# Performance work log

Hardware: AMD Instinct MI355X
Metric: run time of the kernel (lower is better)

The kernel has to match this reference:

```python
import jax, jax.numpy as jnp
import numpy as np

SIM_THRESHOLD = 0.9


def setup_inputs() -> dict:
    key = jax.random.key(0)
    k1, k2 = jax.random.split(key)
    # patches: b * c * num * ws * ws  (b=2, c=8, num=1024, ws=3) -> n = 16384
    patches = jax.random.normal(k1, (2, 8, 1024, 3, 3), dtype=jnp.float32)
    # db: m * ws * ws
    db = jax.random.normal(k2, (16384, 3, 3), dtype=jnp.float32)
    return {"patches": patches, "db": db}


def reference(patches, db):
    ws = patches.shape[-1]
    p = patches.reshape(-1, ws, ws)          # [n, ws, ws]
    n = p.shape[0]
    m = db.shape[0]
    pf = p.reshape(n, -1)                    # [n, ws*ws]
    df = db.reshape(m, -1)                   # [m, ws*ws]
    dot = pf @ df.T                          # [n, m], tiny K=ws*ws -> memory bound
    norm_n = jnp.linalg.norm(pf, axis=1, keepdims=True)   # [n, 1]
    norm_m = jnp.linalg.norm(df, axis=1, keepdims=True)   # [m, 1]
    cos = dot / (norm_n * norm_m.T)          # [n, m] cosine similarity
    # patch kept only if dissimilar to EVERY db entry
    mask = jnp.all(cos < SIM_THRESHOLD, axis=1)            # [n] bool
    # jit-friendly fixed-shape compaction: zero out rejected patches instead of
    # dropping rows (original does db = cat(db, patches[mask]))
    filtered = jnp.where(mask[:, None, None], p, jnp.zeros((), p.dtype))
    return jnp.concatenate([db.reshape(-1, ws, ws), filtered], axis=0)  # [m+n, ws, ws]
```

## Files before the change

### kernel.cpp

```cpp
#include <hip/hip_runtime.h>

#define NPATCH 16384
#define NDB    16384
#define WS9    9
#define KP     16
#define JCH    16
#define CHUNK  (NDB / JCH)
#define TILES  (CHUNK / 32)
#define BAND_LO 0.8998f
#define BAND_HI 0.9002f

typedef short bf16x8 __attribute__((ext_vector_type(8)));
typedef float f32x16 __attribute__((ext_vector_type(16)));

__device__ __forceinline__ float np_norm9(const float* v) {
#pragma clang fp contract(off)
    float q0 = v[0] * v[0], q1 = v[1] * v[1], q2 = v[2] * v[2], q3 = v[3] * v[3];
    float q4 = v[4] * v[4], q5 = v[5] * v[5], q6 = v[6] * v[6], q7 = v[7] * v[7];
    float q8 = v[8] * v[8];
    float s = ((q0 + q1) + (q2 + q3)) + ((q4 + q5) + (q6 + q7));
    s = s + q8;
    return sqrtf(s);
}

__device__ __forceinline__ unsigned enc_f(float f) {
    unsigned u = __float_as_uint(f);
    return (u & 0x80000000u) ? ~u : (u | 0x80000000u);
}
__device__ __forceinline__ float dec_f(unsigned k) {
    return __uint_as_float((k & 0x80000000u) ? (k & 0x7fffffffu) : ~k);
}

__device__ __forceinline__ unsigned short f2bf(float x) {
    unsigned u = __float_as_uint(x);
    return (unsigned short)((u + 0x7fffu + ((u >> 16) & 1u)) >> 16);
}
__device__ __forceinline__ float bf2f(unsigned short h) {
    return __uint_as_float(((unsigned)h) << 16);
}

__global__ __launch_bounds__(256) void k_prep(const float* __restrict__ patches,
                                              const float* __restrict__ db,
                                              unsigned short* __restrict__ pn_hi,
                                              unsigned short* __restrict__ pn_lo,
                                              unsigned short* __restrict__ dn_hi,
                                              unsigned short* __restrict__ dn_lo,
                                              unsigned* __restrict__ maxenc,
                                              int* __restrict__ band_count) {
    int j = blockIdx.x * 256 + threadIdx.x;
    if (j == 0) *band_count = 0;
    maxenc[j] = 0u;

    float d[WS9];
#pragma unroll
    for (int k = 0; k < WS9; k++) d[k] = db[j * WS9 + k];
    float invd = 1.0f / np_norm9(d);
#pragma unroll
    for (int k = 0; k < KP; k++) {
        float v = (k < WS9) ? d[k] * invd : 0.0f;
        unsigned short h = f2bf(v);
        dn_hi[j * KP + k] = h;
        dn_lo[j * KP + k] = f2bf(v - bf2f(h));
    }

    float p[WS9];
#pragma unroll
    for (int k = 0; k < WS9; k++) p[k] = patches[j * WS9 + k];
    float invp = 1.0f / np_norm9(p);
#pragma unroll
    for (int k = 0; k < KP; k++) {
        float v = (k < WS9) ? p[k] * invp : 0.0f;
        unsigned short h = f2bf(v);
        pn_hi[j * KP + k] = h;
        pn_lo[j * KP + k] = f2bf(v - bf2f(h));
    }
}

__global__ __launch_bounds__(256) void k_phase1(const unsigned short* __restrict__ pn_hi,
                                                const unsigned short* __restrict__ pn_lo,
                                                const unsigned short* __restrict__ dn_hi,
                                                const unsigned short* __restrict__ dn_lo,
                                                unsigned* __restrict__ maxenc) {
    int lane = threadIdx.x & 63;
    int wave = threadIdx.x >> 6;
    int col = lane & 31;
    int half = lane >> 5;
    int i0 = blockIdx.x * 256 + wave * 64;

    const bf16x8* Bh = (const bf16x8*)pn_hi;
    const bf16x8* Bl = (const bf16x8*)pn_lo;
    bf16x8 b_hi0 = Bh[(i0 + col) * 2 + half];
    bf16x8 b_lo0 = Bl[(i0 + col) * 2 + half];
    bf16x8 b_hi1 = Bh[(i0 + 32 + col) * 2 + half];
    bf16x8 b_lo1 = Bl[(i0 + 32 + col) * 2 + half];

    int jrow = blockIdx.y * CHUNK + col;
    const bf16x8* Ah = (const bf16x8*)dn_hi + (size_t)jrow * 2 + half;
    const bf16x8* Al = (const bf16x8*)dn_lo + (size_t)jrow * 2 + half;

    f32x16 zc = {0.f,0.f,0.f,0.f,0.f,0.f,0.f,0.f,0.f,0.f,0.f,0.f,0.f,0.f,0.f,0.f};
    float rm0 = -3.0e38f, rm1 = -3.0e38f;

    bf16x8 a_h = Ah[0], a_l = Al[0];
#pragma unroll 2
    for (int t = 0; t < TILES; ++t) {
        bf16x8 a_h_n = a_h, a_l_n = a_l;
        if (t + 1 < TILES) {
            a_h_n = Ah[(t + 1) * 64];
            a_l_n = Al[(t + 1) * 64];
        }
        f32x16 acc0 = __builtin_amdgcn_mfma_f32_32x32x16_bf16(a_h, b_hi0, zc, 0, 0, 0);
        acc0 = __builtin_amdgcn_mfma_f32_32x32x16_bf16(a_h, b_lo0, acc0, 0, 0, 0);
        acc0 = __builtin_amdgcn_mfma_f32_32x32x16_bf16(a_l, b_hi0, acc0, 0, 0, 0);
        f32x16 acc1 = __builtin_amdgcn_mfma_f32_32x32x16_bf16(a_h, b_hi1, zc, 0, 0, 0);
        acc1 = __builtin_amdgcn_mfma_f32_32x32x16_bf16(a_h, b_lo1, acc1, 0, 0, 0);
        acc1 = __builtin_amdgcn_mfma_f32_32x32x16_bf16(a_l, b_hi1, acc1, 0, 0, 0);
#pragma unroll
        for (int r = 0; r < 16; ++r) {
            rm0 = fmaxf(rm0, acc0[r]);
            rm1 = fmaxf(rm1, acc1[r]);
        }
        a_h = a_h_n;
        a_l = a_l_n;
    }
    rm0 = fmaxf(rm0, __shfl_xor(rm0, 32, 64));
    rm1 = fmaxf(rm1, __shfl_xor(rm1, 32, 64));
    unsigned e = half ? enc_f(rm1) : enc_f(rm0);
    int ti = half ? (i0 + 32 + col) : (i0 + col);
    atomicMax(&maxenc[ti], e);
}

__global__ __launch_bounds__(256) void k_combine(const float* __restrict__ patches,
                                                 const float* __restrict__ db,
                                                 const unsigned* __restrict__ maxenc,
                                                 float* __restrict__ out,
                                                 int* __restrict__ band_list,
                                                 int* __restrict__ band_count) {
    int i = blockIdx.x * 256 + threadIdx.x;
#pragma unroll
    for (int k = 0; k < WS9; k++) out[i * WS9 + k] = db[i * WS9 + k];
    float cosmax = dec_f(maxenc[i]);
    if (cosmax >= BAND_LO && cosmax < BAND_HI) {
        int idx = atomicAdd(band_count, 1);
        band_list[idx] = i;
        return;
    }
    int hit = (cosmax >= BAND_HI) ? 1 : 0;
#pragma unroll
    for (int k = 0; k < WS9; k++)
        out[(NDB + i) * WS9 + k] = hit ? 0.0f : patches[i * WS9 + k];
}

__global__ __launch_bounds__(256) void k_phase2(const float* __restrict__ patches,
                                                const float* __restrict__ db,
                                                const int* __restrict__ band_list,
                                                const int* __restrict__ band_count,
                                                float* __restrict__ out) {
    __shared__ float sp[WS9];
    __shared__ float snp;
    __shared__ int shit;
    int nb = *band_count;
    for (int idx = blockIdx.x; idx < nb; idx += gridDim.x) {
        int i = band_list[idx];
        if (threadIdx.x == 0) {
            float p[WS9];
            for (int k = 0; k < WS9; k++) { p[k] = patches[i * WS9 + k]; sp[k] = p[k]; }
            snp = np_norm9(p);
            shit = 0;
        }
        __syncthreads();
        float p[WS9];
#pragma unroll
        for (int k = 0; k < WS9; k++) p[k] = sp[k];
        float npn = snp;
        int hit = 0;
        for (int j = (int)threadIdx.x; j < NDB; j += 256) {
            float d[WS9];
#pragma unroll
            for (int k = 0; k < WS9; k++) d[k] = db[j * WS9 + k];
            float dot = 0.0f;
#pragma unroll
            for (int k = 0; k < WS9; k++) dot = fmaf(p[k], d[k], dot);
            float nd = np_norm9(d);
            float cs = dot / (npn * nd);
            if (!((double)cs < 0.9)) hit = 1;
        }
        if (hit) atomicOr(&shit, 1);
        __syncthreads();
        int m = shit;
        if (threadIdx.x < WS9)
            out[(NDB + i) * WS9 + threadIdx.x] = m ? 0.0f : sp[threadIdx.x];
        __syncthreads();
    }
}

extern "C" void kernel_launch(void* const* d_in, const int* in_sizes, int n_in,
                              void* d_out, int out_size, void* d_ws, size_t ws_size,
                              hipStream_t stream) {
    const float* patches = (const float*)d_in[0];
    const float* db      = (const float*)d_in[1];
    float* out = (float*)d_out;

    char* wsb = (char*)d_ws;
    unsigned*       maxenc     = (unsigned*)wsb;
    int*            band_list  = (int*)(wsb + (size_t)64 * 1024);
    int*            band_count = (int*)(wsb + (size_t)128 * 1024);
    unsigned short* pn_hi      = (unsigned short*)(wsb + (size_t)128 * 1024 + 16);
    unsigned short* pn_lo      = pn_hi + (size_t)NPATCH * KP;
    unsigned short* dn_hi      = pn_lo + (size_t)NPATCH * KP;
    unsigned short* dn_lo      = dn_hi + (size_t)NDB * KP;

    k_prep<<<dim3(NDB / 256), dim3(256), 0, stream>>>(patches, db, pn_hi, pn_lo,
                                                      dn_hi, dn_lo, maxenc, band_count);
    k_phase1<<<dim3(NPATCH / 256, JCH), dim3(256), 0, stream>>>(pn_hi, pn_lo,
                                                                dn_hi, dn_lo, maxenc);
    k_combine<<<dim3(NPATCH / 256), dim3(256), 0, stream>>>(patches, db, maxenc,
                                                            out, band_list, band_count);
    k_phase2<<<dim3(512), dim3(256), 0, stream>>>(patches, db, band_list, band_count, out);
}
```

Baseline: 101.0 us.

## Fuse normalization into phase1 via LDS staging, replace atomics with partial-max buffer

Removes the separate prep kernel: each phase1 block normalizes and splits its db chunk and patch tile into bf16 hi/lo in shared memory, then runs the MFMA loop reading from LDS. Per-chunk row maxima go to a partial buffer instead of atomicMax on encoded floats, which also drops the maxenc init. A single finish kernel reduces the partials and does a vectorized float4 db copy in extra blocks. JCH doubles to 32 and phase2 uses fewer blocks. The cost is that each block recomputes normalization, with redundant work across the grid.

```diff
diff --git a/kernel.cpp b/kernel.cpp
--- a/kernel.cpp
+++ b/kernel.cpp
@@ -4,11 +4,12 @@
 #define NDB    16384
 #define WS9    9
 #define KP     16
-#define JCH    16
+#define JCH    32
 #define CHUNK  (NDB / JCH)
 #define TILES  (CHUNK / 32)
 #define BAND_LO 0.8998f
 #define BAND_HI 0.9002f
+#define COPY_BLOCKS 144
 
 typedef short bf16x8 __attribute__((ext_vector_type(8)));
 typedef float f32x16 __attribute__((ext_vector_type(16)));
@@ -23,14 +24,6 @@
     return sqrtf(s);
 }
 
-__device__ __forceinline__ unsigned enc_f(float f) {
-    unsigned u = __float_as_uint(f);
-    return (u & 0x80000000u) ? ~u : (u | 0x80000000u);
-}
-__device__ __forceinline__ float dec_f(unsigned k) {
-    return __uint_as_float((k & 0x80000000u) ? (k & 0x7fffffffu) : ~k);
-}
-
 __device__ __forceinline__ unsigned short f2bf(float x) {
     unsigned u = __float_as_uint(x);
     return (unsigned short)((u + 0x7fffu + ((u >> 16) & 1u)) >> 16);
@@ -39,76 +32,76 @@
     return __uint_as_float(((unsigned)h) << 16);
 }
 
-__global__ __launch_bounds__(256) void k_prep(const float* __restrict__ patches,
-                                              const float* __restrict__ db,
-                                              unsigned short* __restrict__ pn_hi,
-                                              unsigned short* __restrict__ pn_lo,
-                                              unsigned short* __restrict__ dn_hi,
-                                              unsigned short* __restrict__ dn_lo,
-                                              unsigned* __restrict__ maxenc,
-                                              int* __restrict__ band_count) {
-    int j = blockIdx.x * 256 + threadIdx.x;
-    if (j == 0) *band_count = 0;
-    maxenc[j] = 0u;
-
-    float d[WS9];
-#pragma unroll
-    for (int k = 0; k < WS9; k++) d[k] = db[j * WS9 + k];
-    float invd = 1.0f / np_norm9(d);
+__device__ __forceinline__ void stage_row(const float* __restrict__ src,
+                                          unsigned short* dh, unsigned short* dl) {
+    float v[WS9];
+#pragma unroll
+    for (int k = 0; k < WS9; k++) v[k] = src[k];
+    float inv = 1.0f / np_norm9(v);
+    unsigned short h[KP], l[KP];
 #pragma unroll
     for (int k = 0; k < KP; k++) {
-        float v = (k < WS9) ? d[k] * invd : 0.0f;
-        unsigned short h = f2bf(v);
-        dn_hi[j * KP + k] = h;
-        dn_lo[j * KP + k] = f2bf(v - bf2f(h));
-    }
-
-    float p[WS9];
-#pragma unroll
-    for (int k = 0; k < WS9; k++) p[k] = patches[j * WS9 + k];
-    float invp = 1.0f / np_norm9(p);
-#pragma unroll
-    for (int k = 0; k < KP; k++) {
-        float v = (k < WS9) ? p[k] * invp : 0.0f;
-        unsigned short h = f2bf(v);
-        pn_hi[j * KP + k] = h;
-        pn_lo[j * KP + k] = f2bf(v - bf2f(h));
-    }
-}
-
-__global__ __launch_bounds__(256) void k_phase1(const unsigned short* __restrict__ pn_hi,
-                                                const unsigned short* __restrict__ pn_lo,
-                                                const unsigned short* __restrict__ dn_hi,
-                                                const unsigned short* __restrict__ dn_lo,
-                                                unsigned* __restrict__ maxenc) {
+        float x = (k < WS9) ? v[k] * inv : 0.0f;
+        h[k] = f2bf(x);
+        l[k] = f2bf(x - bf2f(h[k]));
+    }
+    int hw[8], lw[8];
+#pragma unroll
+    for (int k = 0; k < 8; k++) {
+        hw[k] = (int)h[2 * k] | ((int)h[2 * k + 1] << 16);
+        lw[k] = (int)l[2 * k] | ((int)l[2 * k + 1] << 16);
+    }
+    ((int4*)dh)[0] = make_int4(hw[0], hw[1], hw[2], hw[3]);
+    ((int4*)dh)[1] = make_int4(hw[4], hw[5], hw[6], hw[7]);
+    ((int4*)dl)[0] = make_int4(lw[0], lw[1], lw[2], lw[3]);
+    ((int4*)dl)[1] = make_int4(lw[4], lw[5], lw[6], lw[7]);
+}
+
+__global__ __launch_bounds__(256) void k_phase1(const float* __restrict__ patches,
+                                                const float* __restrict__ db,
+                                                float* __restrict__ partial,
+                                                int* __restrict__ band_count) {
+    __shared__ __align__(16) unsigned short s_dnh[CHUNK * KP];
+    __shared__ __align__(16) unsigned short s_dnl[CHUNK * KP];
+    __shared__ __align__(16) unsigned short s_pnh[256 * KP];
+    __shared__ __align__(16) unsigned short s_pnl[256 * KP];
+
+    if (blockIdx.x == 0 && blockIdx.y == 0 && threadIdx.x == 0) *band_count = 0;
+
+    int jbase = blockIdx.y * CHUNK;
+    int ibase = blockIdx.x * 256;
+#pragma unroll
+    for (int rr = 0; rr < CHUNK / 256; rr++) {
+        int r = rr * 256 + threadIdx.x;
+        stage_row(db + (size_t)(jbase + r) * WS9, &s_dnh[r * KP], &s_dnl[r * KP]);
+    }
+    stage_row(patches + (size_t)(ibase + threadIdx.x) * WS9,
+              &s_pnh[threadIdx.x * KP], &s_pnl[threadIdx.x * KP]);
+    __syncthreads();
+
     int lane = threadIdx.x & 63;
     int wave = threadIdx.x >> 6;
     int col = lane & 31;
     int half = lane >> 5;
-    int i0 = blockIdx.x * 256 + wave * 64;
-
-    const bf16x8* Bh = (const bf16x8*)pn_hi;
-    const bf16x8* Bl = (const bf16x8*)pn_lo;
-    bf16x8 b_hi0 = Bh[(i0 + col) * 2 + half];
-    bf16x8 b_lo0 = Bl[(i0 + col) * 2 + half];
-    bf16x8 b_hi1 = Bh[(i0 + 32 + col) * 2 + half];
-    bf16x8 b_lo1 = Bl[(i0 + 32 + col) * 2 + half];
-
-    int jrow = blockIdx.y * CHUNK + col;
-    const bf16x8* Ah = (const bf16x8*)dn_hi + (size_t)jrow * 2 + half;
-    const bf16x8* Al = (const bf16x8*)dn_lo + (size_t)jrow * 2 + half;
+    int i0 = ibase + wave * 64;
+
+    const bf16x8* Ph = (const bf16x8*)s_pnh;
+    const bf16x8* Pl = (const bf16x8*)s_pnl;
+    bf16x8 b_hi0 = Ph[(wave * 64 + col) * 2 + half];
+    bf16x8 b_lo0 = Pl[(wave * 64 + col) * 2 + half];
+    bf16x8 b_hi1 = Ph[(wave * 64 + 32 + col) * 2 + half];
+    bf16x8 b_lo1 = Pl[(wave * 64 + 32 + col) * 2 + half];
+
+    const bf16x8* Ah = (const bf16x8*)s_dnh;
+    const bf16x8* Al = (const bf16x8*)s_dnl;
 
     f32x16 zc = {0.f,0.f,0.f,0.f,0.f,0.f,0.f,0.f,0.f,0.f,0.f,0.f,0.f,0.f,0.f,0.f};
     float rm0 = -3.0e38f, rm1 = -3.0e38f;
 
-    bf16x8 a_h = Ah[0], a_l = Al[0];
 #pragma unroll 2
     for (int t = 0; t < TILES; ++t) {
-        bf16x8 a_h_n = a_h, a_l_n = a_l;
-        if (t + 1 < TILES) {
-            a_h_n = Ah[(t + 1) * 64];
-            a_l_n = Al[(t + 1) * 64];
-        }
+        bf16x8 a_h = Ah[(t * 32 + col) * 2 + half];
+        bf16x8 a_l = Al[(t * 32 + col) * 2 + half];
         f32x16 acc0 = __builtin_amdgcn_mfma_f32_32x32x16_bf16(a_h, b_hi0, zc, 0, 0, 0);
         acc0 = __builtin_amdgcn_mfma_f32_32x32x16_bf16(a_h, b_lo0, acc0, 0, 0, 0);
         acc0 = __builtin_amdgcn_mfma_f32_32x32x16_bf16(a_l, b_hi0, acc0, 0, 0, 0);
@@ -120,26 +113,29 @@
             rm0 = fmaxf(rm0, acc0[r]);
             rm1 = fmaxf(rm1, acc1[r]);
         }
-        a_h = a_h_n;
-        a_l = a_l_n;
     }
     rm0 = fmaxf(rm0, __shfl_xor(rm0, 32, 64));
     rm1 = fmaxf(rm1, __shfl_xor(rm1, 32, 64));
-    unsigned e = half ? enc_f(rm1) : enc_f(rm0);
     int ti = half ? (i0 + 32 + col) : (i0 + col);
-    atomicMax(&maxenc[ti], e);
-}
-
-__global__ __launch_bounds__(256) void k_combine(const float* __restrict__ patches,
-                                                 const float* __restrict__ db,
-                                                 const unsigned* __restrict__ maxenc,
-                                                 float* __restrict__ out,
-                                                 int* __restrict__ band_list,
-                                                 int* __restrict__ band_count) {
-    int i = blockIdx.x * 256 + threadIdx.x;
-#pragma unroll
-    for (int k = 0; k < WS9; k++) out[i * WS9 + k] = db[i * WS9 + k];
-    float cosmax = dec_f(maxenc[i]);
+    partial[(size_t)blockIdx.y * NPATCH + ti] = half ? rm1 : rm0;
+}
+
+__global__ __launch_bounds__(256) void k_finish(const float* __restrict__ patches,
+                                                const float* __restrict__ db,
+                                                const float* __restrict__ partial,
+                                                float* __restrict__ out,
+                                                int* __restrict__ band_list,
+                                                int* __restrict__ band_count) {
+    int b = blockIdx.x;
+    if (b < COPY_BLOCKS) {
+        int e = b * 256 + threadIdx.x;
+        ((float4*)out)[e] = ((const float4*)db)[e];
+        return;
+    }
+    int i = (b - COPY_BLOCKS) * 256 + threadIdx.x;
+    float cosmax = partial[i];
+#pragma unroll
+    for (int c = 1; c < JCH; c++) cosmax = fmaxf(cosmax, partial[(size_t)c * NPATCH + i]);
     if (cosmax >= BAND_LO && cosmax < BAND_HI) {
         int idx = atomicAdd(band_count, 1);
         band_list[idx] = i;
@@ -148,7 +144,7 @@
     int hit = (cosmax >= BAND_HI) ? 1 : 0;
 #pragma unroll
     for (int k = 0; k < WS9; k++)
-        out[(NDB + i) * WS9 + k] = hit ? 0.0f : patches[i * WS9 + k];
+        out[(size_t)(NDB + i) * WS9 + k] = hit ? 0.0f : patches[i * WS9 + k];
 }
 
 __global__ __launch_bounds__(256) void k_phase2(const float* __restrict__ patches,
@@ -189,7 +185,7 @@
         __syncthreads();
         int m = shit;
         if (threadIdx.x < WS9)
-            out[(NDB + i) * WS9 + threadIdx.x] = m ? 0.0f : sp[threadIdx.x];
+            out[(size_t)(NDB + i) * WS9 + threadIdx.x] = m ? 0.0f : sp[threadIdx.x];
         __syncthreads();
     }
 }
@@ -202,19 +198,13 @@
     float* out = (float*)d_out;
 
     char* wsb = (char*)d_ws;
-    unsigned*       maxenc     = (unsigned*)wsb;
-    int*            band_list  = (int*)(wsb + (size_t)64 * 1024);
-    int*            band_count = (int*)(wsb + (size_t)128 * 1024);
-    unsigned short* pn_hi      = (unsigned short*)(wsb + (size_t)128 * 1024 + 16);
-    unsigned short* pn_lo      = pn_hi + (size_t)NPATCH * KP;
-    unsigned short* dn_hi      = pn_lo + (size_t)NPATCH * KP;
-    unsigned short* dn_lo      = dn_hi + (size_t)NDB * KP;
-
-    k_prep<<<dim3(NDB / 256), dim3(256), 0, stream>>>(patches, db, pn_hi, pn_lo,
-                                                      dn_hi, dn_lo, maxenc, band_count);
-    k_phase1<<<dim3(NPATCH / 256, JCH), dim3(256), 0, stream>>>(pn_hi, pn_lo,
-                                                                dn_hi, dn_lo, maxenc);
-    k_combine<<<dim3(NPATCH / 256), dim3(256), 0, stream>>>(patches, db, maxenc,
-                                                            out, band_list, band_count);
-    k_phase2<<<dim3(512), dim3(256), 0, stream>>>(patches, db, band_list, band_count, out);
-}
+    float* partial    = (float*)wsb;
+    int*   band_list  = (int*)(wsb + (size_t)JCH * NPATCH * 4);
+    int*   band_count = (int*)(wsb + (size_t)JCH * NPATCH * 4 + (size_t)NPATCH * 4);
+
+    k_phase1<<<dim3(NPATCH / 256, JCH), dim3(256), 0, stream>>>(patches, db,
+                                                                partial, band_count);
+    k_finish<<<dim3(COPY_BLOCKS + NPATCH / 256), dim3(256), 0, stream>>>(
+        patches, db, partial, out, band_list, band_count);
+    k_phase2<<<dim3(256), dim3(256), 0, stream>>>(patches, db, band_list, band_count, out);
+}
```

Result: faster. 98.32 us (-2.6%).
